# Performance work log

Hardware: AMD Instinct MI355X
Metric: run time of the kernel (lower is better)

The kernel has to match this reference:

```python
import jax, jax.numpy as jnp
import numpy as np

GROUP_SIZES = [5, 5, 5, 5, 5, 5, 4]  # 7 concept groups, sum = 34
LN_EPS = 1e-5


def setup_inputs() -> dict:
    key = jax.random.key(0)
    ks = jax.random.split(key, 12)
    B, N, D, K, P, C, NC, H = 256, 196, 768, 7, 512, 34, 7, 3072
    img_feat_map = jax.random.normal(ks[0], (B, N, D), dtype=jnp.float32)
    # torch: Embedding weight uniform in [-1/K, 1/K]
    vq_codebook = (jax.random.uniform(ks[1], (K, D), dtype=jnp.float32) * 2.0 - 1.0) / K
    agg_codebook = jax.random.normal(ks[2], (K, D), dtype=jnp.float32)
    W1 = jax.random.normal(ks[3], (D, H), dtype=jnp.float32) * 0.02
    b1 = jnp.zeros((H,), dtype=jnp.float32)
    W2 = jax.random.normal(ks[4], (H, D), dtype=jnp.float32) * 0.02
    b2 = jnp.zeros((D,), dtype=jnp.float32)
    ln_gamma = jnp.ones((D,), dtype=jnp.float32)
    ln_beta = jnp.zeros((D,), dtype=jnp.float32)
    W_proj = jax.random.normal(ks[5], (D, P), dtype=jnp.float32) * 0.02
    concept_emb = jax.random.normal(ks[6], (C, P), dtype=jnp.float32)
    concept_emb = concept_emb / jnp.linalg.norm(concept_emb, axis=-1, keepdims=True)
    cls_W = jax.random.normal(ks[7], (C, NC), dtype=jnp.float32) * 0.02
    cls_b = jnp.zeros((NC,), dtype=jnp.float32)
    logit_scale = jnp.float32(100.0)  # detached CLIP logit scale
    return {
        "img_feat_map": img_feat_map, "vq_codebook": vq_codebook,
        "agg_codebook": agg_codebook, "W1": W1, "b1": b1, "W2": W2, "b2": b2,
        "ln_gamma": ln_gamma, "ln_beta": ln_beta, "W_proj": W_proj,
        "concept_emb": concept_emb, "cls_W": cls_W, "cls_b": cls_b,
        "logit_scale": logit_scale,
    }


def _pairwise_sq_dists(x, cb):
    # x: [B, N, D], cb: [K, D] -> [B, N, K]
    x_sq = jnp.sum(x * x, axis=-1, keepdims=True)           # [B, N, 1]
    cb_sq = jnp.sum(cb * cb, axis=-1)                        # [K]
    dot = jnp.einsum("bnd,kd->bnk", x, cb)                  # [B, N, K]
    return x_sq + cb_sq - 2.0 * dot


def _avg_effective_rank(x, threshold=0.99):
    # x: [B, N, D]; per-sample SVD, rank = #{cumsum(S)/sum(S) <= thr}
    S = jnp.linalg.svd(jax.lax.stop_gradient(x), compute_uv=False)  # [B, min(N,D)]
    energy = jnp.cumsum(S, axis=-1) / jnp.sum(S, axis=-1, keepdims=True)
    ranks = jnp.sum(energy <= threshold, axis=-1)
    return jnp.mean(ranks.astype(jnp.float32))


def reference(img_feat_map, vq_codebook, agg_codebook, W1, b1, W2, b2,
              ln_gamma, ln_beta, W_proj, concept_emb, cls_W, cls_b, logit_scale):
    x = img_feat_map  # [B, N, D]

    avg_rank = _avg_effective_rank(x)

    # --- VectorQuantizeAggregator: soft assignment to 7 codes ---
    d_agg = _pairwise_sq_dists(x, agg_codebook)              # [B, N, K]
    soft = jax.nn.softmax(-d_agg, axis=-1)                   # [B, N, K]
    agg = jnp.einsum("bnk,bnd->bkd", soft, x)               # [B, K, D]

    # --- VectorQuantizer: hard argmin + gather (one-hot @ codebook) ---
    d_vq = _pairwise_sq_dists(x, vq_codebook)                # [B, N, K]
    idx = jnp.argmin(d_vq, axis=-1)                          # [B, N] int
    quantized = vq_codebook[idx]                             # [B, N, D] gather == onehot @ cb
    sg = jax.lax.stop_gradient
    codebook_loss = jnp.mean((quantized - sg(x)) ** 2)
    commitment_loss = jnp.mean((sg(quantized) - x) ** 2)
    vq_loss = codebook_loss + 1.0 * commitment_loss

    # --- bridge: FFN -> LayerNorm -> proj -> L2 normalize ---
    h = jax.nn.gelu(agg @ W1 + b1, approximate=False) @ W2 + b2  # [B, K, D]
    mu = jnp.mean(h, axis=-1, keepdims=True)
    var = jnp.mean((h - mu) ** 2, axis=-1, keepdims=True)
    hn = (h - mu) * jax.lax.rsqrt(var + LN_EPS) * ln_gamma + ln_beta
    tok = hn @ W_proj                                        # [B, K, 512]
    tok = tok / jnp.linalg.norm(tok, axis=-1, keepdims=True)

    # --- per-group concept logits: token g vs its concept slice ---
    logits_list = []
    start = 0
    for g, sz in enumerate(GROUP_SIZES):
        ce = concept_emb[start:start + sz]                   # [sz, 512]
        logits_list.append(logit_scale * (tok[:, g, :] @ ce.T))  # [B, sz]
        start += sz
    image_logits = jnp.concatenate(logits_list, axis=-1)     # [B, 34]

    cls_logits = image_logits @ cls_W + cls_b                # [B, 7]
    return (cls_logits, image_logits, vq_loss, avg_rank)
```

## Files before the change

### kernel.cpp

```cpp
#include <hip/hip_runtime.h>
#include <hip/hip_bf16.h>
#include <math.h>

using hbf = __hip_bfloat16;
typedef __bf16 bf16x8 __attribute__((ext_vector_type(8)));
typedef float f32x4 __attribute__((ext_vector_type(4)));

__device__ inline float r16d(float v){
  int x;
  x = __builtin_bit_cast(int, v);
  v += __builtin_bit_cast(float, __builtin_amdgcn_mov_dpp(x, 0x121, 0xf, 0xf, true));
  x = __builtin_bit_cast(int, v);
  v += __builtin_bit_cast(float, __builtin_amdgcn_mov_dpp(x, 0x122, 0xf, 0xf, true));
  x = __builtin_bit_cast(int, v);
  v += __builtin_bit_cast(float, __builtin_amdgcn_mov_dpp(x, 0x124, 0xf, 0xf, true));
  x = __builtin_bit_cast(int, v);
  v += __builtin_bit_cast(float, __builtin_amdgcn_mov_dpp(x, 0x128, 0xf, 0xf, true));
  return v;
}
__device__ inline void r16d4(float& a, float& b, float& c, float& d){
#define R16STAGE(ctl) { \
  int xa=__builtin_bit_cast(int,a), xb=__builtin_bit_cast(int,b); \
  int xc=__builtin_bit_cast(int,c), xd=__builtin_bit_cast(int,d); \
  a += __builtin_bit_cast(float, __builtin_amdgcn_mov_dpp(xa, ctl, 0xf, 0xf, true)); \
  b += __builtin_bit_cast(float, __builtin_amdgcn_mov_dpp(xb, ctl, 0xf, 0xf, true)); \
  c += __builtin_bit_cast(float, __builtin_amdgcn_mov_dpp(xc, ctl, 0xf, 0xf, true)); \
  d += __builtin_bit_cast(float, __builtin_amdgcn_mov_dpp(xd, ctl, 0xf, 0xf, true)); }
  R16STAGE(0x121) R16STAGE(0x122) R16STAGE(0x124) R16STAGE(0x128)
#undef R16STAGE
}
__device__ inline float wred(float v){
  v = r16d(v);
  v += __shfl_xor(v, 16);
  v += __shfl_xor(v, 32);
  return v;
}
__device__ inline float fast_rcp(float x){
  float r; asm("v_rcp_f32 %0, %1" : "=v"(r) : "v"(x)); return r;
}
__device__ inline float d4(const float4& a, const float4& b){
  return a.x*b.x + a.y*b.y + a.z*b.z + a.w*b.w;
}

__global__ void k_init(float* scal){
  if (threadIdx.x < 2) scal[threadIdx.x] = 0.f;
}

__global__ __launch_bounds__(512) void k_dist(const float* __restrict__ x,
    const float* __restrict__ vqcb, const float* __restrict__ agcb,
    hbf* __restrict__ aggbf, float* __restrict__ scal){
  __shared__ float cA[5376];
  __shared__ float cV[5376];
  __shared__ float sqA[7], sqV[7];
  const int tid = threadIdx.x, lane = tid & 63, wave = tid >> 6;
  const int b = blockIdx.x;
  for (int i = tid; i < 5376; i += 512){ cA[i] = agcb[i]; cV[i] = vqcb[i]; }
  __syncthreads();
  {
    int grp = tid >> 4, l16 = tid & 15;
    if (grp < 14){
      const float* s = (grp < 7) ? &cA[grp*768] : &cV[(grp-7)*768];
      float acc = 0.f;
      for (int j = l16; j < 768; j += 16) acc += s[j]*s[j];
      acc = r16d(acc);
      if (l16 == 0){ if (grp < 7) sqA[grp] = acc; else sqV[grp-7] = acc; }
    }
  }
  __syncthreads();
  float sqAr[7], sqVr[7];
#pragma unroll
  for (int k = 0; k < 7; ++k){ sqAr[k] = sqA[k]; sqVr[k] = sqV[k]; }

  float4 aR[7][3];
#pragma unroll
  for (int k = 0; k < 7; ++k)
#pragma unroll
    for (int c = 0; c < 3; ++c) aR[k][c] = make_float4(0.f,0.f,0.f,0.f);
  float loss = 0.f;

  const float* xb = x + (size_t)b*196*768;
  float4 cx0, cx1, cx2, nx0, nx1, nx2;
  { const float* p = xb + (size_t)wave*768 + (lane<<2);
    cx0 = *(const float4*)(p); cx1 = *(const float4*)(p+256); cx2 = *(const float4*)(p+512); }
  for (int it = 0; it < 25; ++it){
    const int n = it*8 + wave;
    const int nn = n + 8;
    if (nn < 196){
      const float* p = xb + (size_t)nn*768 + (lane<<2);
      nx0 = *(const float4*)(p); nx1 = *(const float4*)(p+256); nx2 = *(const float4*)(p+512);
    }
    if (n < 196){
      float xsq = d4(cx0,cx0)+d4(cx1,cx1)+d4(cx2,cx2);
      float dA[7], dV[7];
#pragma unroll
      for (int k = 0; k < 7; ++k){
        const float4* pa = (const float4*)&cA[k*768];
        const float4* pv = (const float4*)&cV[k*768];
        float4 a0 = pa[lane], a1 = pa[64+lane], a2 = pa[128+lane];
        float4 q0 = pv[lane], q1 = pv[64+lane], q2 = pv[128+lane];
        dA[k] = d4(cx0,a0)+d4(cx1,a1)+d4(cx2,a2);
        dV[k] = d4(cx0,q0)+d4(cx1,q1)+d4(cx2,q2);
      }
      xsq = wred(xsq);
#pragma unroll
      for (int k = 0; k < 7; ++k){ dA[k] = wred(dA[k]); dV[k] = wred(dV[k]); }
      float lg[7], mx = -1e30f;
#pragma unroll
      for (int k = 0; k < 7; ++k){ lg[k] = 2.f*dA[k] - sqAr[k]; mx = fmaxf(mx, lg[k]); }
      float pr[7], ssum = 0.f;
#pragma unroll
      for (int k = 0; k < 7; ++k){ pr[k] = expf(lg[k]-mx); ssum += pr[k]; }
      const float inv = 1.f/ssum;
      float mn = 1e30f;
#pragma unroll
      for (int k = 0; k < 7; ++k) mn = fminf(mn, sqVr[k] - 2.f*dV[k]);
      loss += xsq + mn;
#pragma unroll
      for (int k = 0; k < 7; ++k){
        const float w = pr[k]*inv;
        aR[k][0].x += w*cx0.x; aR[k][0].y += w*cx0.y; aR[k][0].z += w*cx0.z; aR[k][0].w += w*cx0.w;
        aR[k][1].x += w*cx1.x; aR[k][1].y += w*cx1.y; aR[k][1].z += w*cx1.z; aR[k][1].w += w*cx1.w;
        aR[k][2].x += w*cx2.x; aR[k][2].y += w*cx2.y; aR[k][2].z += w*cx2.z; aR[k][2].w += w*cx2.w;
      }
    }
    cx0 = nx0; cx1 = nx1; cx2 = nx2;
  }
  __syncthreads();
  for (int i = tid; i < 5376; i += 512) cA[i] = 0.f;
  __syncthreads();
  for (int w = 0; w < 8; ++w){
    if (wave == w){
#pragma unroll
      for (int k = 0; k < 7; ++k)
#pragma unroll
        for (int c = 0; c < 3; ++c){
          float* p = &cA[k*768 + c*256 + (lane<<2)];
          p[0] += aR[k][c].x; p[1] += aR[k][c].y; p[2] += aR[k][c].z; p[3] += aR[k][c].w;
        }
    }
    __syncthreads();
  }
  for (int i = tid; i < 5376; i += 512) aggbf[(size_t)b*5376 + i] = __float2bfloat16(cA[i]);
  if (lane == 0) atomicAdd(&scal[0], loss);
}

__global__ __launch_bounds__(512) void k_gram(const float* __restrict__ x, float* __restrict__ G){
  __shared__ hbf Xs[208*104];
  const int tid = threadIdx.x, lane = tid & 63, wave = tid >> 6;
  const int b = blockIdx.x;
  const int l15 = lane & 15;
  const int fr0 = wave, fr1 = wave + 8;
  const bool f1 = (fr1 < 13);
  f32x4 acc0[13] = {};
  f32x4 acc1[13] = {};
  const float* xb = x + (size_t)b*196*768;
  for (int kc = 0; kc < 8; ++kc){
    __syncthreads();
    for (int u = tid; u < 4992; u += 512){
      const int r = u / 24, c4 = u - r*24;
      ushort4 val;
      if (r < 196){
        float4 f = *(const float4*)(xb + (size_t)r*768 + kc*96 + c4*4);
        hbf t0 = __float2bfloat16(f.x), t1 = __float2bfloat16(f.y);
        hbf t2 = __float2bfloat16(f.z), t3 = __float2bfloat16(f.w);
        val.x = *(const unsigned short*)&t0; val.y = *(const unsigned short*)&t1;
        val.z = *(const unsigned short*)&t2; val.w = *(const unsigned short*)&t3;
      } else { val.x = 0; val.y = 0; val.z = 0; val.w = 0; }
      *(ushort4*)&Xs[r*104 + c4*4] = val;
    }
    __syncthreads();
#pragma unroll
    for (int kk = 0; kk < 3; ++kk){
      const int ko = kk*32 + (lane>>4)*8;
      bf16x8 a0 = *(const bf16x8*)&Xs[(fr0*16 + l15)*104 + ko];
      bf16x8 a1 = f1 ? *(const bf16x8*)&Xs[(fr1*16 + l15)*104 + ko] : a0;
#pragma unroll
      for (int fc = 0; fc < 13; ++fc){
        bf16x8 bb = *(const bf16x8*)&Xs[(fc*16 + l15)*104 + ko];
        acc0[fc] = __builtin_amdgcn_mfma_f32_16x16x32_bf16(a0, bb, acc0[fc], 0, 0, 0);
        if (f1) acc1[fc] = __builtin_amdgcn_mfma_f32_16x16x32_bf16(a1, bb, acc1[fc], 0, 0, 0);
      }
    }
  }
  const size_t gb = (size_t)b*38416;
  const int cr = (lane>>4)*4;
#pragma unroll
  for (int fc = 0; fc < 13; ++fc){
    const int gc = fc*16 + l15;
    if (gc < 196){
#pragma unroll
      for (int r = 0; r < 4; ++r){
        const int gr = fr0*16 + cr + r;
        if (gr < 196) G[gb + (size_t)gr*196 + gc] = acc0[fc][r];
      }
      if (f1){
#pragma unroll
        for (int r = 0; r < 4; ++r){
          const int gr = fr1*16 + cr + r;
          if (gr < 196) G[gb + (size_t)gr*196 + gc] = acc1[fc][r];
        }
      }
    }
  }
}

#define ESTR 196
#define FOLD4v(FR, V0) { FR.x = (oc==0)? (V0) : FR.x; FR.y = (oc==1)? (V0) : FR.y; \
                         FR.z = (oc==2)? (V0) : FR.z; FR.w = (oc==3)? (V0) : FR.w; }
#define VH(COLC, BASE, OUT) { \
  const int col_ = (COLC) + jc4; \
  const float4 xv_ = *(const float4*)(rowk + col_); \
  float4 vp_; \
  if (col_ > (BASE)){ vp_ = xv_; } \
  else if (col_ + 3 <= (BASE)){ vp_ = make_float4(0.f,0.f,0.f,0.f); } \
  else { vp_.x = 0.f; \
         vp_.y = (col_+1 > (BASE)) ? xv_.y : 0.f; \
         vp_.z = (col_+2 > (BASE)) ? xv_.z : 0.f; \
         vp_.w = xv_.w; } \
  OUT = vp_; sig += vp_.x*vp_.x + vp_.y*vp_.y + vp_.z*vp_.z + vp_.w*vp_.w; }

__global__ __launch_bounds__(1024) void k_eigen(const float* __restrict__ G, float* __restrict__ scal){
  extern __shared__ float S[];
  float* A    = S;
  float* ww1  = S + 38496;
  float* ww2  = S + 38752;
  float* dd   = S + 39008;
  float* ee   = S + 39208;
  float* e2   = S + 39408;
  float* red2 = S + 39608;
  float* red2b= S + 39624;
  const int n = 196;
  const int tid = threadIdx.x, lane = tid & 63, wave = tid >> 6;
  const int grp = lane >> 4, c16 = lane & 15;
  const int jc4 = c16 << 2;
  const int rbase = (wave << 2) + grp;
  const int b = blockIdx.x;
  {
    const float4* Gv = (const float4*)(G + (size_t)b*38416);
    float4* Av = (float4*)A;
    for (int u = tid; u < 9604; u += 1024) Av[u] = Gv[u];
    if (tid < 592) S[38416 + tid] = 0.f;
  }
  __syncthreads();
  for (int k = 0; k <= 130; k += 2){
    const int base1 = k + 1, base2 = k + 2;
    const int m1 = n - 1 - k, m2 = n - 2 - k;
    const float* rowk  = &A[(size_t)k*ESTR];
    const float* rowk1 = &A[(size_t)base1*ESTR];
    if (tid == 0 && k > 0){
      ww1[k-1] = 0.f; ww1[k] = 0.f;
      ww2[k]   = 0.f; ww2[k+1] = 0.f;
    }
    const float x01 = rowk[base1];
    float4 v1f0, v1f1, v1f2, v1f3;
    float sig = 0.f;
    VH(0,   base1, v1f0)
    VH(64,  base1, v1f1)
    VH(128, base1, v1f2)
    { float4 vp = make_float4(0.f,0.f,0.f,0.f);
      if (c16 == 0){ vp = *(const float4*)(rowk + 192);
        sig += vp.x*vp.x + vp.y*vp.y + vp.z*vp.z + vp.w*vp.w; }
      v1f3 = vp; }
    sig = r16d(sig);
    float tau1 = 0.f, v01 = 0.f, alpha1 = x01;
    if (sig > 1e-20f){
      const float mu = sqrtf(x01*x01 + sig);
      alpha1 = (x01 > 0.f) ? -mu : mu;
      v01 = x01 - alpha1;
      tau1 = 2.f/(sig + v01*v01);
    }
    if (tid == 0) ee[k] = alpha1;
    if (c16 == ((base1 >> 2) & 15)){
      const int oc = base1 & 3, op = base1 >> 6;
      if (op == 0){ FOLD4v(v1f0, v01) } else if (op == 1){ FOLD4v(v1f1, v01) } else { FOLD4v(v1f2, v01) }
    }
    const int p0 = base1 >> 6;
    const int i0r = rbase, i1r = 64 + rbase, i2r = 128 + rbase, i3r = 192 + rbase;
    {
      float a0c = 0.f, a1c = 0.f, a2c = 0.f, a3c = 0.f;
#define MV1(IV, ACC) { \
      if ((IV) < m1){ \
        const float* Ar = &A[(size_t)(base1+(IV))*ESTR]; \
        if (0 >= p0) ACC += d4(*(const float4*)(Ar + jc4), v1f0); \
        if (1 >= p0) ACC += d4(*(const float4*)(Ar + 64 + jc4), v1f1); \
        if (2 >= p0) ACC += d4(*(const float4*)(Ar + 128 + jc4), v1f2); \
        if (c16 == 0) ACC += d4(*(const float4*)(Ar + 192), v1f3); } }
      MV1(i0r, a0c) MV1(i1r, a1c) MV1(i2r, a2c) MV1(i3r, a3c)
#undef MV1
      r16d4(a0c, a1c, a2c, a3c);
      float cp = 0.f;
#define CP1(IV, ACC) { \
      if ((IV) < m1){ \
        const float wr_ = tau1*(ACC); \
        const float vr_ = ((IV) == 0) ? v01 : rowk[base1+(IV)]; \
        cp += vr_*wr_; \
        if (c16 == 0) ww1[base1+(IV)] = wr_; } }
      CP1(i0r, a0c) CP1(i1r, a1c) CP1(i2r, a2c) CP1(i3r, a3c)
#undef CP1
      cp += __shfl_xor(cp, 16);
      cp += __shfl_xor(cp, 32);
      if (lane == 0) red2[wave] = cp;
    }
    __syncthreads();
    float c21, w1head, tau2 = 0.f, v02 = 0.f;
    float4 w1f0, w1f1, w1f2, w1f3;
    float4 v2f0, v2f1, v2f2, v2f3;
    {
      const float4* r2 = (const float4*)red2;
      const float4 q0 = r2[0], q1 = r2[1], q2 = r2[2], q3 = r2[3];
      const float vtw = (q0.x+q0.y+q0.z+q0.w) + (q1.x+q1.y+q1.z+q1.w)
                      + (q2.x+q2.y+q2.z+q2.w) + (q3.x+q3.y+q3.z+q3.w);
      c21 = 0.5f*tau1*vtw;
      w1head = ww1[base1] - c21*v01;
      if (tid == 0) A[(size_t)base1*ESTR + base1] = rowk1[base1] - 2.f*v01*w1head;
#define W1F(COLC, VF, OUT) { \
      const float4 t4 = *(const float4*)(ww1 + (COLC) + jc4); \
      OUT.x = t4.x - c21*VF.x; OUT.y = t4.y - c21*VF.y; \
      OUT.z = t4.z - c21*VF.z; OUT.w = t4.w - c21*VF.w; }
      W1F(0,   v1f0, w1f0)
      W1F(64,  v1f1, w1f1)
      W1F(128, v1f2, w1f2)
      { float4 wp = make_float4(0.f,0.f,0.f,0.f);
        if (c16 == 0){ const float4 t4 = *(const float4*)(ww1 + 192);
          wp.x = t4.x - c21*v1f3.x; wp.y = t4.y - c21*v1f3.y;
          wp.z = t4.z - c21*v1f3.z; wp.w = t4.w - c21*v1f3.w; }
        w1f3 = wp; }
#undef W1F
      float sig2 = 0.f;
#define V2F(COLC, VF1, WF1, OUT) { \
      const int col_ = (COLC) + jc4; \
      const float4 r1_ = *(const float4*)(rowk1 + col_); \
      float4 rp_; \
      rp_.x = r1_.x - v01*WF1.x - w1head*VF1.x; \
      rp_.y = r1_.y - v01*WF1.y - w1head*VF1.y; \
      rp_.z = r1_.z - v01*WF1.z - w1head*VF1.z; \
      rp_.w = r1_.w - v01*WF1.w - w1head*VF1.w; \
      float4 vp_; \
      if (col_ > base2){ vp_ = rp_; } \
      else if (col_ + 3 <= base2){ vp_ = make_float4(0.f,0.f,0.f,0.f); } \
      else { vp_.x = 0.f; \
             vp_.y = (col_+1 > base2) ? rp_.y : 0.f; \
             vp_.z = (col_+2 > base2) ? rp_.z : 0.f; \
             vp_.w = rp_.w; } \
      OUT = vp_; sig2 += vp_.x*vp_.x + vp_.y*vp_.y + vp_.z*vp_.z + vp_.w*vp_.w; }
      V2F(0,   v1f0, w1f0, v2f0)
      V2F(64,  v1f1, w1f1, v2f1)
      V2F(128, v1f2, w1f2, v2f2)
      { float4 vp = make_float4(0.f,0.f,0.f,0.f);
        if (c16 == 0){ const float4 r1_ = *(const float4*)(rowk1 + 192);
          vp.x = r1_.x - v01*w1f3.x - w1head*v1f3.x;
          vp.y = r1_.y - v01*w1f3.y - w1head*v1f3.y;
          vp.z = r1_.z - v01*w1f3.z - w1head*v1f3.z;
// ... 178 lines not shown
          w4_2.x = t4.x - c2*v4_2.x; w4_2.y = t4.y - c2*v4_2.y; w4_2.z = t4.z - c2*v4_2.z; w4_2.w = t4.w - c2*v4_2.w; }
        if (c16 == 0){
          const float4 t4 = *(const float4*)(ww + 192);
          w4_3.x = t4.x - c2*v4_3.x; w4_3.y = t4.y - c2*v4_3.y; w4_3.z = t4.z - c2*v4_3.z; w4_3.w = t4.w - c2*v4_3.w; }
#pragma unroll
        for (int t = 0; t < 16; ++t){
          const int i_ = (t << 2) + grp;
          if (i_ < m){
            const float vi = vrT[t];
            const float wi = wrT[t] - c2*vi;
            float* Ar = &A[(size_t)(base+i_)*ESTR];
            float4 a = *(const float4*)(Ar + 128 + jc4);
            a.x -= vi*w4_2.x + wi*v4_2.x; a.y -= vi*w4_2.y + wi*v4_2.y;
            a.z -= vi*w4_2.z + wi*v4_2.z; a.w -= vi*w4_2.w + wi*v4_2.w;
            *(float4*)(Ar + 128 + jc4) = a;
            if (c16 == 0){
              float4 a3 = *(const float4*)(Ar + 192);
              a3.x -= vi*w4_3.x + wi*v4_3.x; a3.y -= vi*w4_3.y + wi*v4_3.y;
              a3.z -= vi*w4_3.z + wi*v4_3.z; a3.w -= vi*w4_3.w + wi*v4_3.w;
              *(float4*)(Ar + 192) = a3;
            }
          }
        }
        __threadfence_block();
      }
    }
  }
  __syncthreads();
  if (tid < n) dd[tid] = A[(size_t)tid*ESTR + tid];
  if (tid == 0) ee[n-2] = A[(size_t)(n-1)*ESTR + (n-2)];
  __syncthreads();
  if (tid < n-1) e2[tid] = ee[tid]*ee[tid];
  __syncthreads();
  float lo = 1e30f, hi = -1e30f;
  if (tid < n){
    const float rr = ((tid > 0) ? fabsf(ee[tid-1]) : 0.f) + ((tid < n-1) ? fabsf(ee[tid]) : 0.f);
    lo = dd[tid] - rr; hi = dd[tid] + rr;
  }
  {
    float l2 = lo, h2 = hi;
#pragma unroll
    for (int o = 32; o > 0; o >>= 1){
      l2 = fminf(l2, __shfl_xor(l2, o));
      h2 = fmaxf(h2, __shfl_xor(h2, o));
    }
    if (lane == 0){ ww1[wave] = l2; red2[wave] = h2; }
  }
  __syncthreads();
  float glo = ww1[0], ghi = red2[0];
#pragma unroll
  for (int w2 = 1; w2 < 16; ++w2){ glo = fminf(glo, ww1[w2]); ghi = fmaxf(ghi, red2[w2]); }
  __syncthreads();
  float sv = 0.f;
  if (tid < n){
    float lob = glo, hib = ghi;
    for (int it2 = 0; it2 < 18; ++it2){
      const float mid = 0.5f*(lob + hib);
      float q = dd[0] - mid;
      int cnt = (q < 0.f) ? 1 : 0;
      for (int i = 1; i < n; ++i){
        const float r = fast_rcp(q);
        q = (dd[i] - mid) - e2[i-1]*r;
        q = (fabsf(q) < 1e-6f) ? -1e-6f : q;
        cnt += (q < 0.f) ? 1 : 0;
      }
      if (cnt <= tid) lob = mid; else hib = mid;
    }
    sv = sqrtf(fmaxf(0.5f*(lob + hib), 0.f));
  }
  __syncthreads();
  if (tid < n) ww1[tid] = sv;
  __syncthreads();
  if (tid == 0){
    float tot = 0.f;
    for (int i = 0; i < n; ++i) tot += ww1[i];
    const float thr = 0.99f*tot;
    float cs = 0.f; int rank = 0;
    for (int i = n-1; i >= 0; --i){ cs += ww1[i]; rank += (cs <= thr) ? 1 : 0; }
    atomicAdd(&scal[1], (float)rank);
  }
}

__global__ __launch_bounds__(256) void k_tr(const float* __restrict__ in, hbf* __restrict__ outp,
                                            int Rr, int Cc){
  __shared__ float t[32][33];
  const int tid = threadIdx.x;
  const int lc = tid & 31, lr = tid >> 5;
  const int c0 = blockIdx.x*32, r0 = blockIdx.y*32;
#pragma unroll
  for (int i = 0; i < 4; ++i)
    t[lr + i*8][lc] = in[(size_t)(r0 + lr + i*8)*Cc + c0 + lc];
  __syncthreads();
#pragma unroll
  for (int i = 0; i < 4; ++i)
    outp[(size_t)(c0 + lr + i*8)*Rr + r0 + lc] = __float2bfloat16(t[lc][lr + i*8]);
}

template<int EPI>
__global__ __launch_bounds__(512) void k_gemm128(const hbf* __restrict__ Aa, const hbf* __restrict__ Bb,
    const float* __restrict__ bias, void* __restrict__ outp, int Ni, int Ki){
  __shared__ hbf As[128*72];
  __shared__ hbf Bs[128*72];
  const int tid = threadIdx.x, lane = tid & 63, wave = tid >> 6;
  const int row0 = blockIdx.y*128, col0 = blockIdx.x*128;
  const int m0 = (wave >> 2)*64, n0 = (wave & 3)*32;
  const int l15 = lane & 15, lk = (lane >> 4)*8;
  const int sr = tid >> 3, sc = (tid & 7)*8;
  f32x4 acc[4][2] = {};
  for (int kt = 0; kt < Ki; kt += 64){
    __syncthreads();
    *(uint4*)&As[sr*72 + sc]      = *(const uint4*)&Aa[(size_t)(row0+sr)*Ki + kt + sc];
    *(uint4*)&As[(sr+64)*72 + sc] = *(const uint4*)&Aa[(size_t)(row0+sr+64)*Ki + kt + sc];
    *(uint4*)&Bs[sr*72 + sc]      = *(const uint4*)&Bb[(size_t)(col0+sr)*Ki + kt + sc];
    *(uint4*)&Bs[(sr+64)*72 + sc] = *(const uint4*)&Bb[(size_t)(col0+sr+64)*Ki + kt + sc];
    __syncthreads();
#pragma unroll
    for (int kk = 0; kk < 2; ++kk){
      const int ko = kk*32 + lk;
      bf16x8 b0 = *(const bf16x8*)&Bs[(n0 + l15)*72 + ko];
      bf16x8 b1 = *(const bf16x8*)&Bs[(n0 + 16 + l15)*72 + ko];
#pragma unroll
      for (int mi = 0; mi < 4; ++mi){
        bf16x8 a = *(const bf16x8*)&As[(m0 + mi*16 + l15)*72 + ko];
        acc[mi][0] = __builtin_amdgcn_mfma_f32_16x16x32_bf16(a, b0, acc[mi][0], 0, 0, 0);
        acc[mi][1] = __builtin_amdgcn_mfma_f32_16x16x32_bf16(a, b1, acc[mi][1], 0, 0, 0);
      }
    }
  }
  const int cr = (lane >> 4)*4;
#pragma unroll
  for (int mi = 0; mi < 4; ++mi){
#pragma unroll
    for (int ni = 0; ni < 2; ++ni){
      const int gcol = col0 + n0 + ni*16 + l15;
#pragma unroll
      for (int r = 0; r < 4; ++r){
        const int grow = row0 + m0 + mi*16 + cr + r;
        float v = acc[mi][ni][r];
        if (EPI == 1){
          v += bias[gcol];
          v = 0.5f*v*(1.f + erff(v*0.70710678118654752f));
          ((hbf*)outp)[(size_t)grow*Ni + gcol] = __float2bfloat16(v);
        } else if (EPI == 2){
          v += bias[gcol];
          ((float*)outp)[(size_t)grow*Ni + gcol] = v;
        } else {
          ((float*)outp)[(size_t)grow*Ni + gcol] = v;
        }
      }
    }
  }
}

template<int EPI>
__global__ __launch_bounds__(256) void k_gemm(const hbf* __restrict__ Aa, const hbf* __restrict__ Bb,
    const float* __restrict__ bias, void* __restrict__ outp, int Mi, int Ni, int Ki){
  __shared__ hbf As[64*72];
  __shared__ hbf Bs[64*72];
  const int tid = threadIdx.x, lane = tid & 63, wave = tid >> 6;
  const int row0 = blockIdx.y*64, col0 = blockIdx.x*64;
  const int m0 = (wave >> 1)*32, n0 = (wave & 1)*32;
  const int l15 = lane & 15, lk = (lane >> 4)*8;
  const int sr = tid >> 3, sc = (tid & 7)*8;
  f32x4 acc00 = {}, acc01 = {}, acc10 = {}, acc11 = {};
  for (int kt = 0; kt < Ki; kt += 64){
    __syncthreads();
    *(uint4*)&As[sr*72 + sc]        = *(const uint4*)&Aa[(size_t)(row0+sr)*Ki + kt + sc];
    *(uint4*)&As[(sr+32)*72 + sc]   = *(const uint4*)&Aa[(size_t)(row0+sr+32)*Ki + kt + sc];
    *(uint4*)&Bs[sr*72 + sc]        = *(const uint4*)&Bb[(size_t)(col0+sr)*Ki + kt + sc];
    *(uint4*)&Bs[(sr+32)*72 + sc]   = *(const uint4*)&Bb[(size_t)(col0+sr+32)*Ki + kt + sc];
    __syncthreads();
#pragma unroll
    for (int kk = 0; kk < 2; ++kk){
      const int ko = kk*32 + lk;
      bf16x8 a0 = *(const bf16x8*)&As[(m0 + l15)*72 + ko];
      bf16x8 a1 = *(const bf16x8*)&As[(m0 + 16 + l15)*72 + ko];
      bf16x8 b0 = *(const bf16x8*)&Bs[(n0 + l15)*72 + ko];
      bf16x8 b1 = *(const bf16x8*)&Bs[(n0 + 16 + l15)*72 + ko];
      acc00 = __builtin_amdgcn_mfma_f32_16x16x32_bf16(a0, b0, acc00, 0, 0, 0);
      acc01 = __builtin_amdgcn_mfma_f32_16x16x32_bf16(a0, b1, acc01, 0, 0, 0);
      acc10 = __builtin_amdgcn_mfma_f32_16x16x32_bf16(a1, b0, acc10, 0, 0, 0);
      acc11 = __builtin_amdgcn_mfma_f32_16x16x32_bf16(a1, b1, acc11, 0, 0, 0);
    }
  }
  const int cr = (lane >> 4)*4;
#pragma unroll
  for (int i = 0; i < 2; ++i){
#pragma unroll
    for (int j = 0; j < 2; ++j){
      f32x4 av = (i == 0) ? ((j == 0) ? acc00 : acc01) : ((j == 0) ? acc10 : acc11);
      const int gcol = col0 + n0 + j*16 + l15;
#pragma unroll
      for (int r = 0; r < 4; ++r){
        const int grow = row0 + m0 + i*16 + cr + r;
        float v = av[r];
        if (EPI == 1){
          v += bias[gcol];
          v = 0.5f*v*(1.f + erff(v*0.70710678118654752f));
          ((hbf*)outp)[(size_t)grow*Ni + gcol] = __float2bfloat16(v);
        } else if (EPI == 2){
          v += bias[gcol];
          ((float*)outp)[(size_t)grow*Ni + gcol] = v;
        } else {
          ((float*)outp)[(size_t)grow*Ni + gcol] = v;
        }
      }
    }
  }
}

__global__ __launch_bounds__(256) void k_ln(const float* __restrict__ h, const float* __restrict__ gam,
    const float* __restrict__ bet, hbf* __restrict__ hn){
  const int tid = threadIdx.x, lane = tid & 63, wave = tid >> 6;
  const int row = blockIdx.x*4 + wave;
  const float* hr = h + (size_t)row*768;
  const int off = lane*4;
  float4 v0 = *(const float4*)(hr + off);
  float4 v1 = *(const float4*)(hr + 256 + off);
  float4 v2 = *(const float4*)(hr + 512 + off);
  float s = v0.x+v0.y+v0.z+v0.w + v1.x+v1.y+v1.z+v1.w + v2.x+v2.y+v2.z+v2.w;
  s = wred(s);
  const float mu = s*(1.f/768.f);
  float q = 0.f;
  q += (v0.x-mu)*(v0.x-mu); q += (v0.y-mu)*(v0.y-mu); q += (v0.z-mu)*(v0.z-mu); q += (v0.w-mu)*(v0.w-mu);
  q += (v1.x-mu)*(v1.x-mu); q += (v1.y-mu)*(v1.y-mu); q += (v1.z-mu)*(v1.z-mu); q += (v1.w-mu)*(v1.w-mu);
  q += (v2.x-mu)*(v2.x-mu); q += (v2.y-mu)*(v2.y-mu); q += (v2.z-mu)*(v2.z-mu); q += (v2.w-mu)*(v2.w-mu);
  q = wred(q);
  const float rs = 1.f/sqrtf(q*(1.f/768.f) + 1e-5f);
  float4 g0 = *(const float4*)(gam + off), g1 = *(const float4*)(gam + 256 + off), g2 = *(const float4*)(gam + 512 + off);
  float4 t0 = *(const float4*)(bet + off), t1 = *(const float4*)(bet + 256 + off), t2 = *(const float4*)(bet + 512 + off);
  hbf* o = hn + (size_t)row*768;
  o[off+0] = __float2bfloat16((v0.x-mu)*rs*g0.x + t0.x);
  o[off+1] = __float2bfloat16((v0.y-mu)*rs*g0.y + t0.y);
  o[off+2] = __float2bfloat16((v0.z-mu)*rs*g0.z + t0.z);
  o[off+3] = __float2bfloat16((v0.w-mu)*rs*g0.w + t0.w);
  o[256+off+0] = __float2bfloat16((v1.x-mu)*rs*g1.x + t1.x);
  o[256+off+1] = __float2bfloat16((v1.y-mu)*rs*g1.y + t1.y);
  o[256+off+2] = __float2bfloat16((v1.z-mu)*rs*g1.z + t1.z);
  o[256+off+3] = __float2bfloat16((v1.w-mu)*rs*g1.w + t1.w);
  o[512+off+0] = __float2bfloat16((v2.x-mu)*rs*g2.x + t2.x);
  o[512+off+1] = __float2bfloat16((v2.y-mu)*rs*g2.y + t2.y);
  o[512+off+2] = __float2bfloat16((v2.z-mu)*rs*g2.z + t2.z);
  o[512+off+3] = __float2bfloat16((v2.w-mu)*rs*g2.w + t2.w);
}

__global__ __launch_bounds__(256) void k_head(const float* __restrict__ tok, const float* __restrict__ ce,
    const float* __restrict__ clsW, const float* __restrict__ clsb, const float* __restrict__ lgs,
    float* __restrict__ out){
  __shared__ float tkn[7*512];
  __shared__ float il[40];
  const int tid = threadIdx.x, lane = tid & 63, wave = tid >> 6;
  const int b = blockIdx.x;
  const float ls = lgs[0];
  for (int g = wave; g < 7; g += 4){
    const float* tr = tok + (size_t)(b*7 + g)*512;
    float4 u0 = *(const float4*)(tr + (lane<<3));
    float4 u1 = *(const float4*)(tr + (lane<<3) + 4);
    float s = d4(u0,u0) + d4(u1,u1);
    s = wred(s);
    const float inv = 1.f/sqrtf(s);
    float* dst = &tkn[g*512 + (lane<<3)];
    dst[0] = u0.x*inv; dst[1] = u0.y*inv; dst[2] = u0.z*inv; dst[3] = u0.w*inv;
    dst[4] = u1.x*inv; dst[5] = u1.y*inv; dst[6] = u1.z*inv; dst[7] = u1.w*inv;
  }
  __syncthreads();
  for (int c = wave; c < 34; c += 4){
    const int g = (c < 30) ? (c/5) : 6;
    const float* tp = &tkn[g*512 + (lane<<3)];
    const float* cp = ce + (size_t)c*512 + (lane<<3);
    float s = tp[0]*cp[0] + tp[1]*cp[1] + tp[2]*cp[2] + tp[3]*cp[3]
            + tp[4]*cp[4] + tp[5]*cp[5] + tp[6]*cp[6] + tp[7]*cp[7];
    s = wred(s);
    if (lane == 0){
      const float v = ls*s;
      il[c] = v;
      out[1792 + b*34 + c] = v;
    }
  }
  __syncthreads();
  if (tid < 7){
    float s = clsb[tid];
    for (int c = 0; c < 34; ++c) s += il[c]*clsW[c*7 + tid];
    out[b*7 + tid] = s;
  }
}

__global__ void k_fin(const float* __restrict__ scal, float* __restrict__ out){
  if (threadIdx.x == 0){
    out[10496] = 2.f*scal[0]/(float)(256*196*768);
    out[10497] = scal[1]*(1.f/256.f);
  }
}

extern "C" void kernel_launch(void* const* d_in, const int* in_sizes, int n_in,
                              void* d_out, int out_size, void* d_ws, size_t ws_size,
                              hipStream_t stream) {
  (void)in_sizes; (void)n_in; (void)out_size; (void)ws_size;
  const float* x    = (const float*)d_in[0];
  const float* vqcb = (const float*)d_in[1];
  const float* agcb = (const float*)d_in[2];
  const float* W1   = (const float*)d_in[3];
  const float* b1   = (const float*)d_in[4];
  const float* W2   = (const float*)d_in[5];
  const float* b2   = (const float*)d_in[6];
  const float* gam  = (const float*)d_in[7];
  const float* bet  = (const float*)d_in[8];
  const float* Wp   = (const float*)d_in[9];
  const float* ce   = (const float*)d_in[10];
  const float* clsW = (const float*)d_in[11];
  const float* clsb = (const float*)d_in[12];
  const float* lgs  = (const float*)d_in[13];
  float* out = (float*)d_out;
  char* w = (char*)d_ws;

  float* scal  = (float*)w;
  float* G     = (float*)(w + 256);
  hbf*   aggbf = (hbf*)(w + 39338240ULL);
  hbf*   W1t   = (hbf*)(w + 42090752ULL);
  hbf*   W2t   = (hbf*)(w + 46809344ULL);
  hbf*   Wpt   = (hbf*)(w + 51527936ULL);
  hbf*   h1    = (hbf*)(w + 256);
  float* hbuf  = (float*)(w + 256 + 16777216ULL);
  hbf*   hn    = (hbf*)(w + 256 + 25165824ULL);
  float* tok   = (float*)(w + 256 + 29360128ULL);

  k_init<<<dim3(1), dim3(64), 0, stream>>>(scal);
  k_dist<<<dim3(256), dim3(512), 0, stream>>>(x, vqcb, agcb, aggbf, scal);
  k_gram<<<dim3(256), dim3(512), 0, stream>>>(x, G);
  const int EIG_SMEM = 39640*4;
  hipFuncSetAttribute((const void*)k_eigen, hipFuncAttributeMaxDynamicSharedMemorySize, EIG_SMEM);
  k_eigen<<<dim3(256), dim3(1024), EIG_SMEM, stream>>>(G, scal);
  k_tr<<<dim3(96,24), dim3(256), 0, stream>>>(W1, W1t, 768, 3072);
  k_tr<<<dim3(24,96), dim3(256), 0, stream>>>(W2, W2t, 3072, 768);
  k_tr<<<dim3(16,24), dim3(256), 0, stream>>>(Wp, Wpt, 768, 512);
  k_gemm128<1><<<dim3(24,14), dim3(512), 0, stream>>>(aggbf, W1t, b1, (void*)h1, 3072, 768);
  k_gemm<2><<<dim3(12,28), dim3(256), 0, stream>>>(h1, W2t, b2, (void*)hbuf, 1792, 768, 3072);
  k_ln<<<dim3(448), dim3(256), 0, stream>>>(hbuf, gam, bet, hn);
  k_gemm<3><<<dim3(8,28), dim3(256), 0, stream>>>(hn, Wpt, nullptr, (void*)tok, 1792, 512, 768);
  k_head<<<dim3(256), dim3(256), 0, stream>>>(tok, ce, clsW, clsb, lgs, out);
  k_fin<<<dim3(1), dim3(64), 0, stream>>>(scal, out);
}
```

Measured before the change: 1.017 ms.

## Fuse distance and Gram kernels; use 128-tile GEMM for W2 and projection

```diff
diff --git a/kernel.cpp b/kernel.cpp
--- a/kernel.cpp
+++ b/kernel.cpp
@@ -46,158 +46,156 @@
   if (threadIdx.x < 2) scal[threadIdx.x] = 0.f;
 }
 
-__global__ __launch_bounds__(512) void k_dist(const float* __restrict__ x,
+__global__ __launch_bounds__(512) void k_dg(const float* __restrict__ x,
     const float* __restrict__ vqcb, const float* __restrict__ agcb,
-    hbf* __restrict__ aggbf, float* __restrict__ scal){
-  __shared__ float cA[5376];
-  __shared__ float cV[5376];
+    hbf* __restrict__ aggbf, float* __restrict__ scal, float* __restrict__ G){
+  __shared__ __align__(16) char smem[43264];
   __shared__ float sqA[7], sqV[7];
   const int tid = threadIdx.x, lane = tid & 63, wave = tid >> 6;
   const int b = blockIdx.x;
-  for (int i = tid; i < 5376; i += 512){ cA[i] = agcb[i]; cV[i] = vqcb[i]; }
-  __syncthreads();
+  const float* xb = x + (size_t)b*196*768;
   {
-    int grp = tid >> 4, l16 = tid & 15;
-    if (grp < 14){
-      const float* s = (grp < 7) ? &cA[grp*768] : &cV[(grp-7)*768];
-      float acc = 0.f;
-      for (int j = l16; j < 768; j += 16) acc += s[j]*s[j];
-      acc = r16d(acc);
-      if (l16 == 0){ if (grp < 7) sqA[grp] = acc; else sqV[grp-7] = acc; }
-    }
-  }
-  __syncthreads();
-  float sqAr[7], sqVr[7];
-#pragma unroll
-  for (int k = 0; k < 7; ++k){ sqAr[k] = sqA[k]; sqVr[k] = sqV[k]; }
-
-  float4 aR[7][3];
-#pragma unroll
-  for (int k = 0; k < 7; ++k)
-#pragma unroll
-    for (int c = 0; c < 3; ++c) aR[k][c] = make_float4(0.f,0.f,0.f,0.f);
-  float loss = 0.f;
-
-  const float* xb = x + (size_t)b*196*768;
-  float4 cx0, cx1, cx2, nx0, nx1, nx2;
-  { const float* p = xb + (size_t)wave*768 + (lane<<2);
-    cx0 = *(const float4*)(p); cx1 = *(const float4*)(p+256); cx2 = *(const float4*)(p+512); }
-  for (int it = 0; it < 25; ++it){
-    const int n = it*8 + wave;
-    const int nn = n + 8;
-    if (nn < 196){
-      const float* p = xb + (size_t)nn*768 + (lane<<2);
-      nx0 = *(const float4*)(p); nx1 = *(const float4*)(p+256); nx2 = *(const float4*)(p+512);
-    }
-    if (n < 196){
-      float xsq = d4(cx0,cx0)+d4(cx1,cx1)+d4(cx2,cx2);
-      float dA[7], dV[7];
-#pragma unroll
-      for (int k = 0; k < 7; ++k){
-        const float4* pa = (const float4*)&cA[k*768];
-        const float4* pv = (const float4*)&cV[k*768];
-        float4 a0 = pa[lane], a1 = pa[64+lane], a2 = pa[128+lane];
-        float4 q0 = pv[lane], q1 = pv[64+lane], q2 = pv[128+lane];
-        dA[k] = d4(cx0,a0)+d4(cx1,a1)+d4(cx2,a2);
-        dV[k] = d4(cx0,q0)+d4(cx1,q1)+d4(cx2,q2);
-      }
-      xsq = wred(xsq);
-#pragma unroll
-      for (int k = 0; k < 7; ++k){ dA[k] = wred(dA[k]); dV[k] = wred(dV[k]); }
-      float lg[7], mx = -1e30f;
-#pragma unroll
-      for (int k = 0; k < 7; ++k){ lg[k] = 2.f*dA[k] - sqAr[k]; mx = fmaxf(mx, lg[k]); }
-      float pr[7], ssum = 0.f;
-#pragma unroll
-      for (int k = 0; k < 7; ++k){ pr[k] = expf(lg[k]-mx); ssum += pr[k]; }
-      const float inv = 1.f/ssum;
-      float mn = 1e30f;
-#pragma unroll
-      for (int k = 0; k < 7; ++k) mn = fminf(mn, sqVr[k] - 2.f*dV[k]);
-      loss += xsq + mn;
-#pragma unroll
-      for (int k = 0; k < 7; ++k){
-        const float w = pr[k]*inv;
-        aR[k][0].x += w*cx0.x; aR[k][0].y += w*cx0.y; aR[k][0].z += w*cx0.z; aR[k][0].w += w*cx0.w;
-        aR[k][1].x += w*cx1.x; aR[k][1].y += w*cx1.y; aR[k][1].z += w*cx1.z; aR[k][1].w += w*cx1.w;
-        aR[k][2].x += w*cx2.x; aR[k][2].y += w*cx2.y; aR[k][2].z += w*cx2.z; aR[k][2].w += w*cx2.w;
-      }
-    }
-    cx0 = nx0; cx1 = nx1; cx2 = nx2;
-  }
-  __syncthreads();
-  for (int i = tid; i < 5376; i += 512) cA[i] = 0.f;
-  __syncthreads();
-  for (int w = 0; w < 8; ++w){
-    if (wave == w){
-#pragma unroll
-      for (int k = 0; k < 7; ++k)
-#pragma unroll
-        for (int c = 0; c < 3; ++c){
-          float* p = &cA[k*768 + c*256 + (lane<<2)];
-          p[0] += aR[k][c].x; p[1] += aR[k][c].y; p[2] += aR[k][c].z; p[3] += aR[k][c].w;
+    float* cA = (float*)smem;
+    float* cV = cA + 5376;
+    for (int i = tid; i < 5376; i += 512){ cA[i] = agcb[i]; cV[i] = vqcb[i]; }
+    __syncthreads();
+    {
+      int grp = tid >> 4, l16 = tid & 15;
+      if (grp < 14){
+        const float* s = (grp < 7) ? &cA[grp*768] : &cV[(grp-7)*768];
+        float acc = 0.f;
+        for (int j = l16; j < 768; j += 16) acc += s[j]*s[j];
+        acc = r16d(acc);
+        if (l16 == 0){ if (grp < 7) sqA[grp] = acc; else sqV[grp-7] = acc; }
+      }
+    }
+    __syncthreads();
+    float sqAr[7], sqVr[7];
+#pragma unroll
+    for (int k = 0; k < 7; ++k){ sqAr[k] = sqA[k]; sqVr[k] = sqV[k]; }
+    float4 aR[7][3];
+#pragma unroll
+    for (int k = 0; k < 7; ++k)
+#pragma unroll
+      for (int c = 0; c < 3; ++c) aR[k][c] = make_float4(0.f,0.f,0.f,0.f);
+    float loss = 0.f;
+    float4 cx0, cx1, cx2, nx0, nx1, nx2;
+    { const float* p = xb + (size_t)wave*768 + (lane<<2);
+      cx0 = *(const float4*)(p); cx1 = *(const float4*)(p+256); cx2 = *(const float4*)(p+512); }
+    for (int it = 0; it < 25; ++it){
+      const int n = it*8 + wave;
+      const int nn = n + 8;
+      if (nn < 196){
+        const float* p = xb + (size_t)nn*768 + (lane<<2);
+        nx0 = *(const float4*)(p); nx1 = *(const float4*)(p+256); nx2 = *(const float4*)(p+512);
+      }
+      if (n < 196){
+        float xsq = d4(cx0,cx0)+d4(cx1,cx1)+d4(cx2,cx2);
+        float dA[7], dV[7];
+#pragma unroll
+        for (int k = 0; k < 7; ++k){
+          const float4* pa = (const float4*)&cA[k*768];
+          const float4* pv = (const float4*)&cV[k*768];
+          float4 a0 = pa[lane], a1 = pa[64+lane], a2 = pa[128+lane];
+          float4 q0 = pv[lane], q1 = pv[64+lane], q2 = pv[128+lane];
+          dA[k] = d4(cx0,a0)+d4(cx1,a1)+d4(cx2,a2);
+          dV[k] = d4(cx0,q0)+d4(cx1,q1)+d4(cx2,q2);
         }
-    }
-    __syncthreads();
-  }
-  for (int i = tid; i < 5376; i += 512) aggbf[(size_t)b*5376 + i] = __float2bfloat16(cA[i]);
-  if (lane == 0) atomicAdd(&scal[0], loss);
-}
-
-__global__ __launch_bounds__(512) void k_gram(const float* __restrict__ x, float* __restrict__ G){
-  __shared__ hbf Xs[208*104];
-  const int tid = threadIdx.x, lane = tid & 63, wave = tid >> 6;
-  const int b = blockIdx.x;
-  const int l15 = lane & 15;
-  const int fr0 = wave, fr1 = wave + 8;
-  const bool f1 = (fr1 < 13);
-  f32x4 acc0[13] = {};
-  f32x4 acc1[13] = {};
-  const float* xb = x + (size_t)b*196*768;
-  for (int kc = 0; kc < 8; ++kc){
-    __syncthreads();
-    for (int u = tid; u < 4992; u += 512){
-      const int r = u / 24, c4 = u - r*24;
-      ushort4 val;
-      if (r < 196){
-        float4 f = *(const float4*)(xb + (size_t)r*768 + kc*96 + c4*4);
-        hbf t0 = __float2bfloat16(f.x), t1 = __float2bfloat16(f.y);
-        hbf t2 = __float2bfloat16(f.z), t3 = __float2bfloat16(f.w);
-        val.x = *(const unsigned short*)&t0; val.y = *(const unsigned short*)&t1;
-        val.z = *(const unsigned short*)&t2; val.w = *(const unsigned short*)&t3;
-      } else { val.x = 0; val.y = 0; val.z = 0; val.w = 0; }
-      *(ushort4*)&Xs[r*104 + c4*4] = val;
-    }
-    __syncthreads();
-#pragma unroll
-    for (int kk = 0; kk < 3; ++kk){
-      const int ko = kk*32 + (lane>>4)*8;
-      bf16x8 a0 = *(const bf16x8*)&Xs[(fr0*16 + l15)*104 + ko];
-      bf16x8 a1 = f1 ? *(const bf16x8*)&Xs[(fr1*16 + l15)*104 + ko] : a0;
-#pragma unroll
-      for (int fc = 0; fc < 13; ++fc){
-        bf16x8 bb = *(const bf16x8*)&Xs[(fc*16 + l15)*104 + ko];
-        acc0[fc] = __builtin_amdgcn_mfma_f32_16x16x32_bf16(a0, bb, acc0[fc], 0, 0, 0);
-        if (f1) acc1[fc] = __builtin_amdgcn_mfma_f32_16x16x32_bf16(a1, bb, acc1[fc], 0, 0, 0);
-      }
-    }
-  }
-  const size_t gb = (size_t)b*38416;
-  const int cr = (lane>>4)*4;
-#pragma unroll
-  for (int fc = 0; fc < 13; ++fc){
-    const int gc = fc*16 + l15;
-    if (gc < 196){
-#pragma unroll
-      for (int r = 0; r < 4; ++r){
-        const int gr = fr0*16 + cr + r;
-        if (gr < 196) G[gb + (size_t)gr*196 + gc] = acc0[fc][r];
-      }
-      if (f1){
+        xsq = wred(xsq);
+#pragma unroll
+        for (int k = 0; k < 7; ++k){ dA[k] = wred(dA[k]); dV[k] = wred(dV[k]); }
+        float lg[7], mx = -1e30f;
+#pragma unroll
+        for (int k = 0; k < 7; ++k){ lg[k] = 2.f*dA[k] - sqAr[k]; mx = fmaxf(mx, lg[k]); }
+        float pr[7], ssum = 0.f;
+#pragma unroll
+        for (int k = 0; k < 7; ++k){ pr[k] = expf(lg[k]-mx); ssum += pr[k]; }
+        const float inv = 1.f/ssum;
+        float mn = 1e30f;
+#pragma unroll
+        for (int k = 0; k < 7; ++k) mn = fminf(mn, sqVr[k] - 2.f*dV[k]);
+        loss += xsq + mn;
+#pragma unroll
+        for (int k = 0; k < 7; ++k){
+          const float w = pr[k]*inv;
+          aR[k][0].x += w*cx0.x; aR[k][0].y += w*cx0.y; aR[k][0].z += w*cx0.z; aR[k][0].w += w*cx0.w;
+          aR[k][1].x += w*cx1.x; aR[k][1].y += w*cx1.y; aR[k][1].z += w*cx1.z; aR[k][1].w += w*cx1.w;
+          aR[k][2].x += w*cx2.x; aR[k][2].y += w*cx2.y; aR[k][2].z += w*cx2.z; aR[k][2].w += w*cx2.w;
+        }
+      }
+      cx0 = nx0; cx1 = nx1; cx2 = nx2;
+    }
+    __syncthreads();
+    for (int i = tid; i < 5376; i += 512) cA[i] = 0.f;
+    __syncthreads();
+    for (int w = 0; w < 8; ++w){
+      if (wave == w){
+#pragma unroll
+        for (int k = 0; k < 7; ++k)
+#pragma unroll
+          for (int c = 0; c < 3; ++c){
+            float* p = &cA[k*768 + c*256 + (lane<<2)];
+            p[0] += aR[k][c].x; p[1] += aR[k][c].y; p[2] += aR[k][c].z; p[3] += aR[k][c].w;
+          }
+      }
+      __syncthreads();
+    }
+    for (int i = tid; i < 5376; i += 512) aggbf[(size_t)b*5376 + i] = __float2bfloat16(cA[i]);
+    if (lane == 0) atomicAdd(&scal[0], loss);
+    __syncthreads();
+  }
+  {
+    hbf* Xs = (hbf*)smem;
+    const int l15 = lane & 15;
+    const int fr0 = wave, fr1 = wave + 8;
+    const bool f1 = (fr1 < 13);
+    f32x4 acc0[13] = {};
+    f32x4 acc1[13] = {};
+    for (int kc = 0; kc < 8; ++kc){
+      __syncthreads();
+      for (int u = tid; u < 4992; u += 512){
+        const int r = u / 24, c4 = u - r*24;
+        ushort4 val;
+        if (r < 196){
+          float4 f = *(const float4*)(xb + (size_t)r*768 + kc*96 + c4*4);
+          hbf t0 = __float2bfloat16(f.x), t1 = __float2bfloat16(f.y);
+          hbf t2 = __float2bfloat16(f.z), t3 = __float2bfloat16(f.w);
+          val.x = *(const unsigned short*)&t0; val.y = *(const unsigned short*)&t1;
+          val.z = *(const unsigned short*)&t2; val.w = *(const unsigned short*)&t3;
+        } else { val.x = 0; val.y = 0; val.z = 0; val.w = 0; }
+        *(ushort4*)&Xs[r*104 + c4*4] = val;
+      }
+      __syncthreads();
+#pragma unroll
+      for (int kk = 0; kk < 3; ++kk){
+        const int ko = kk*32 + (lane>>4)*8;
+        bf16x8 a0 = *(const bf16x8*)&Xs[(fr0*16 + l15)*104 + ko];
+        bf16x8 a1 = f1 ? *(const bf16x8*)&Xs[(fr1*16 + l15)*104 + ko] : a0;
+#pragma unroll
+        for (int fc = 0; fc < 13; ++fc){
+          bf16x8 bb = *(const bf16x8*)&Xs[(fc*16 + l15)*104 + ko];
+          acc0[fc] = __builtin_amdgcn_mfma_f32_16x16x32_bf16(a0, bb, acc0[fc], 0, 0, 0);
+          if (f1) acc1[fc] = __builtin_amdgcn_mfma_f32_16x16x32_bf16(a1, bb, acc1[fc], 0, 0, 0);
+        }
+      }
+    }
+    const size_t gb = (size_t)b*38416;
+    const int cr = (lane>>4)*4;
+#pragma unroll
+    for (int fc = 0; fc < 13; ++fc){
+      const int gc = fc*16 + l15;
+      if (gc < 196){
 #pragma unroll
         for (int r = 0; r < 4; ++r){
-          const int gr = fr1*16 + cr + r;
-          if (gr < 196) G[gb + (size_t)gr*196 + gc] = acc1[fc][r];
+          const int gr = fr0*16 + cr + r;
+          if (gr < 196) G[gb + (size_t)gr*196 + gc] = acc0[fc][r];
+        }
+        if (f1){
+#pragma unroll
+          for (int r = 0; r < 4; ++r){
+            const int gr = fr1*16 + cr + r;
+            if (gr < 196) G[gb + (size_t)gr*196 + gc] = acc1[fc][r];
+          }
         }
       }
     }
@@ -682,63 +680,6 @@
   }
 }
 
-template<int EPI>
-__global__ __launch_bounds__(256) void k_gemm(const hbf* __restrict__ Aa, const hbf* __restrict__ Bb,
-    const float* __restrict__ bias, void* __restrict__ outp, int Mi, int Ni, int Ki){
-  __shared__ hbf As[64*72];
-  __shared__ hbf Bs[64*72];
-  const int tid = threadIdx.x, lane = tid & 63, wave = tid >> 6;
-  const int row0 = blockIdx.y*64, col0 = blockIdx.x*64;
-  const int m0 = (wave >> 1)*32, n0 = (wave & 1)*32;
-  const int l15 = lane & 15, lk = (lane >> 4)*8;
-  const int sr = tid >> 3, sc = (tid & 7)*8;
-  f32x4 acc00 = {}, acc01 = {}, acc10 = {}, acc11 = {};
-  for (int kt = 0; kt < Ki; kt += 64){
-    __syncthreads();
-    *(uint4*)&As[sr*72 + sc]        = *(const uint4*)&Aa[(size_t)(row0+sr)*Ki + kt + sc];
-    *(uint4*)&As[(sr+32)*72 + sc]   = *(const uint4*)&Aa[(size_t)(row0+sr+32)*Ki + kt + sc];
-    *(uint4*)&Bs[sr*72 + sc]        = *(const uint4*)&Bb[(size_t)(col0+sr)*Ki + kt + sc];
-    *(uint4*)&Bs[(sr+32)*72 + sc]   = *(const uint4*)&Bb[(size_t)(col0+sr+32)*Ki + kt + sc];
-    __syncthreads();
-#pragma unroll
-    for (int kk = 0; kk < 2; ++kk){
-      const int ko = kk*32 + lk;
-      bf16x8 a0 = *(const bf16x8*)&As[(m0 + l15)*72 + ko];
-      bf16x8 a1 = *(const bf16x8*)&As[(m0 + 16 + l15)*72 + ko];
-      bf16x8 b0 = *(const bf16x8*)&Bs[(n0 + l15)*72 + ko];
-      bf16x8 b1 = *(const bf16x8*)&Bs[(n0 + 16 + l15)*72 + ko];
-      acc00 = __builtin_amdgcn_mfma_f32_16x16x32_bf16(a0, b0, acc00, 0, 0, 0);
-      acc01 = __builtin_amdgcn_mfma_f32_16x16x32_bf16(a0, b1, acc01, 0, 0, 0);
-      acc10 = __builtin_amdgcn_mfma_f32_16x16x32_bf16(a1, b0, acc10, 0, 0, 0);
-      acc11 = __builtin_amdgcn_mfma_f32_16x16x32_bf16(a1, b1, acc11, 0, 0, 0);
-    }
-  }
-  const int cr = (lane >> 4)*4;
-#pragma unroll
-  for (int i = 0; i < 2; ++i){
-#pragma unroll
-    for (int j = 0; j < 2; ++j){
-      f32x4 av = (i == 0) ? ((j == 0) ? acc00 : acc01) : ((j == 0) ? acc10 : acc11);
-      const int gcol = col0 + n0 + j*16 + l15;
-#pragma unroll
-      for (int r = 0; r < 4; ++r){
-        const int grow = row0 + m0 + i*16 + cr + r;
-        float v = av[r];
-        if (EPI == 1){
-          v += bias[gcol];
-          v = 0.5f*v*(1.f + erff(v*0.70710678118654752f));
-          ((hbf*)outp)[(size_t)grow*Ni + gcol] = __float2bfloat16(v);
-        } else if (EPI == 2){
-          v += bias[gcol];
-          ((float*)outp)[(size_t)grow*Ni + gcol] = v;
-        } else {
-          ((float*)outp)[(size_t)grow*Ni + gcol] = v;
-        }
-      }
-    }
-  }
-}
-
 __global__ __launch_bounds__(256) void k_ln(const float* __restrict__ h, const float* __restrict__ gam,
     const float* __restrict__ bet, hbf* __restrict__ hn){
   const int tid = threadIdx.x, lane = tid & 63, wave = tid >> 6;
@@ -855,8 +796,7 @@
   float* tok   = (float*)(w + 256 + 29360128ULL);
 
   k_init<<<dim3(1), dim3(64), 0, stream>>>(scal);
-  k_dist<<<dim3(256), dim3(512), 0, stream>>>(x, vqcb, agcb, aggbf, scal);
-  k_gram<<<dim3(256), dim3(512), 0, stream>>>(x, G);
+  k_dg<<<dim3(256), dim3(512), 0, stream>>>(x, vqcb, agcb, aggbf, scal, G);
   const int EIG_SMEM = 39640*4;
   hipFuncSetAttribute((const void*)k_eigen, hipFuncAttributeMaxDynamicSharedMemorySize, EIG_SMEM);
   k_eigen<<<dim3(256), dim3(1024), EIG_SMEM, stream>>>(G, scal);
@@ -864,9 +804,9 @@
   k_tr<<<dim3(24,96), dim3(256), 0, stream>>>(W2, W2t, 3072, 768);
   k_tr<<<dim3(16,24), dim3(256), 0, stream>>>(Wp, Wpt, 768, 512);
   k_gemm128<1><<<dim3(24,14), dim3(512), 0, stream>>>(aggbf, W1t, b1, (void*)h1, 3072, 768);
-  k_gemm<2><<<dim3(12,28), dim3(256), 0, stream>>>(h1, W2t, b2, (void*)hbuf, 1792, 768, 3072);
+  k_gemm128<2><<<dim3(6,14), dim3(512), 0, stream>>>(h1, W2t, b2, (void*)hbuf, 768, 3072);
   k_ln<<<dim3(448), dim3(256), 0, stream>>>(hbuf, gam, bet, hn);
-  k_gemm<3><<<dim3(8,28), dim3(256), 0, stream>>>(hn, Wpt, nullptr, (void*)tok, 1792, 512, 768);
+  k_gemm128<3><<<dim3(4,14), dim3(512), 0, stream>>>(hn, Wpt, nullptr, (void*)tok, 512, 768);
   k_head<<<dim3(256), dim3(256), 0, stream>>>(tok, ce, clsW, clsb, lgs, out);
   k_fin<<<dim3(1), dim3(64), 0, stream>>>(scal, out);
 }
```

Measured after the change: 1.032 ms. Within noise of the previous version (+1.5%).
